# Kernel optimization log

Hardware: AMD Instinct MI355X
Metric: run time of the kernel (lower is better)

## Reference

```python
import jax, jax.numpy as jnp
import numpy as np

E = 192      # embed_dim
DI = 384     # d_inner = 2*E (mamba default expand=2)
S = 16       # d_state
R = 12       # dt_rank = ceil(E/16)
DEPTH = 4
STRIDE = 4
P = 400      # num_patches = 1600/4
NC = 20
BATCH = 32
EPS = 1e-5


def _rmsnorm(x, w):
    x = x.astype(jnp.float32)
    return x * jax.lax.rsqrt(jnp.mean(x * x, axis=-1, keepdims=True) + EPS) * w


def _mamba_mixer(h, in_w, cw, cb, xpw, dtw, dtb, a_log, d_skip, ow):
    # h: [B, L, E]
    Bsz, Ln, _ = h.shape
    xz = jnp.einsum('ble,de->bld', h, in_w)            # [B,L,2*DI]
    xm, z = xz[..., :DI], xz[..., DI:]
    # causal depthwise conv1d, kernel 4 (left pad 3, truncate to L)
    xp = jnp.pad(xm, ((0, 0), (3, 0), (0, 0)))
    xc = sum(xp[:, k:k + Ln, :] * cw[:, k] for k in range(4)) + cb
    xc = jax.nn.silu(xc)
    xdb = jnp.einsum('bld,rd->blr', xc, xpw)           # [B,L,R+2S]
    dt = jax.nn.softplus(jnp.einsum('blr,dr->bld', xdb[..., :R], dtw) + dtb)
    Bm = xdb[..., R:R + S]
    Cm = xdb[..., R + S:]
    A = -jnp.exp(a_log)                                # [DI,S]

    def step(hst, inp):
        dt_t, b_t, c_t, u_t = inp                      # [B,DI],[B,S],[B,S],[B,DI]
        dA = jnp.exp(dt_t[:, :, None] * A)             # [B,DI,S]
        hst = dA * hst + (dt_t * u_t)[:, :, None] * b_t[:, None, :]
        y_t = jnp.einsum('bdn,bn->bd', hst, c_t)
        return hst, y_t

    h0 = jnp.zeros((Bsz, DI, S), xc.dtype)
    xs = (dt.transpose(1, 0, 2), Bm.transpose(1, 0, 2), Cm.transpose(1, 0, 2), xc.transpose(1, 0, 2))
    _, ys = jax.lax.scan(step, h0, xs)
    y = ys.transpose(1, 0, 2) + xc * d_skip
    y = y * jax.nn.silu(z)
    return jnp.einsum('bld,ed->ble', y, ow)


def _forward(imgs, patch_w, patch_b, cls_token, pos_embed, cnn_w, cnn_b, norm_w,
             in_proj_w, conv_w, conv_b, x_proj_w, dt_proj_w, dt_proj_b, A_log, D,
             out_proj_w, norm_f_w, head_w, head_b):
    Bsz = imgs.shape[0]
    # StrideEmbed: conv1d kernel=stride=4 == reshape + matmul
    x = imgs.reshape(Bsz, P, STRIDE)
    x = jnp.einsum('blk,ek->ble', x, patch_w[:, 0, :]) + patch_b   # [B,P,E]
    x = x + pos_embed[:, :-1, :]
    # depthwise conv1d k=3 pad=1 over length
    xp = jnp.pad(x, ((0, 0), (1, 1), (0, 0)))
    x = sum(xp[:, k:k + P, :] * cnn_w[:, 0, k] for k in range(3)) + cnn_b
    cls = cls_token + pos_embed[:, -1, :]                           # [1,1,E]
    x = jnp.concatenate([x, jnp.broadcast_to(cls, (Bsz, 1, E))], axis=1)  # [B,401,E]

    hidden = x
    residual = None
    for i in range(DEPTH):
        residual = hidden if residual is None else residual + hidden
        hn = _rmsnorm(residual, norm_w[i])
        hidden = _mamba_mixer(hn, in_proj_w[i], conv_w[i], conv_b[i], x_proj_w[i],
                              dt_proj_w[i], dt_proj_b[i], A_log[i], D[i], out_proj_w[i])
    out = _rmsnorm(hidden + residual, norm_f_w)
    v_sem = out[:, -1, :]
    return v_sem @ head_w.T + head_b


def setup_inputs() -> dict:
    key = jax.random.key(0)
    ks = jax.random.split(key, 12)
    n = lambda k, shp, s=0.02: jax.random.normal(k, shp, dtype=jnp.float32) * s
    return {
        'imgs': jax.random.normal(ks[0], (BATCH, 1, 40, 40), jnp.float32),
        'patch_w': n(ks[1], (E, 1, STRIDE), 0.3),
        'patch_b': jnp.zeros((E,), jnp.float32),
        'cls_token': n(ks[2], (1, 1, E)),
        'pos_embed': n(ks[3], (1, P + 1, E)),
        'cnn_w': n(ks[4], (E, 1, 3), 0.3),
        'cnn_b': jnp.zeros((E,), jnp.float32),
        'norm_w': jnp.ones((DEPTH, E), jnp.float32),
        'in_proj_w': n(ks[5], (DEPTH, 2 * DI, E), 0.05),
        'conv_w': n(ks[6], (DEPTH, DI, 4), 0.3),
        'conv_b': jnp.zeros((DEPTH, DI), jnp.float32),
        'x_proj_w': n(ks[7], (DEPTH, R + 2 * S, DI), 0.05),
        'dt_proj_w': n(ks[8], (DEPTH, DI, R), 0.3),
        'dt_proj_b': jnp.log(jnp.expm1(jax.random.uniform(ks[9], (DEPTH, DI), minval=0.001, maxval=0.1))),
        'A_log': jnp.log(jnp.broadcast_to(jnp.arange(1, S + 1, dtype=jnp.float32), (DEPTH, DI, S))),
        'D': jnp.ones((DEPTH, DI), jnp.float32),
        'out_proj_w': n(ks[10], (DEPTH, E, DI), 0.05),
        'norm_f_w': jnp.ones((E,), jnp.float32),
        'head_w': n(ks[11], (NC, E)),
        'head_b': jnp.zeros((NC,), jnp.float32),
    }


def reference(imgs, patch_w, patch_b, cls_token, pos_embed, cnn_w, cnn_b, norm_w,
              in_proj_w, conv_w, conv_b, x_proj_w, dt_proj_w, dt_proj_b, A_log, D,
              out_proj_w, norm_f_w, head_w, head_b):
    return _forward(imgs, patch_w, patch_b, cls_token, pos_embed, cnn_w, cnn_b, norm_w,
                    in_proj_w, conv_w, conv_b, x_proj_w, dt_proj_w, dt_proj_b, A_log, D,
                    out_proj_w, norm_f_w, head_w, head_b)
```

## Files before the change

kernel.cpp:

```cpp
#include <hip/hip_runtime.h>
#include <math.h>

#define E 192
#define DI 384
#define S 16
#define R 12
#define DEPTH 4
#define P 400
#define NC 20
#define BATCH 32
#define L 401
#define NTOK (BATCH * L)
#define CH 64
#define NCH 7

using short8 = __attribute__((ext_vector_type(8))) short;
using float4v = __attribute__((ext_vector_type(4))) float;

__device__ __forceinline__ float siluf(float x) {
    return x / (1.f + __expf(-x));
}
__device__ __forceinline__ float softplusf(float x) {
    return (x > 20.f) ? x : log1pf(__expf(x));
}
__device__ __forceinline__ unsigned short f2bf(float x) {
    unsigned int u = __float_as_uint(x);
    unsigned int r = 0x7fffu + ((u >> 16) & 1u);
    return (unsigned short)((u + r) >> 16);
}

__global__ void k_embed(const float* __restrict__ imgs, const float* __restrict__ patch_w,
                        const float* __restrict__ patch_b, const float* __restrict__ cls_token,
                        const float* __restrict__ pos_embed, const float* __restrict__ cnn_w,
                        const float* __restrict__ cnn_b, float* __restrict__ resid) {
    int idx = blockIdx.x * blockDim.x + threadIdx.x;
    if (idx >= NTOK * E) return;
    int e = idx % E;
    int bl = idx / E;
    int l = bl % L;
    int b = bl / L;
    float out;
    if (l == P) {
        out = cls_token[e] + pos_embed[(size_t)P * E + e];
    } else {
        float w0 = patch_w[e * 4 + 0], w1 = patch_w[e * 4 + 1];
        float w2 = patch_w[e * 4 + 2], w3 = patch_w[e * 4 + 3];
        float pb = patch_b[e];
        const float* ib = imgs + (size_t)b * 1600;
        auto xe = [&](int ll) -> float {
            const float* ip = ib + ll * 4;
            return ip[0] * w0 + ip[1] * w1 + ip[2] * w2 + ip[3] * w3 + pb +
                   pos_embed[(size_t)ll * E + e];
        };
        float c0 = cnn_w[e * 3 + 0], c1 = cnn_w[e * 3 + 1], c2 = cnn_w[e * 3 + 2];
        float acc = cnn_b[e] + xe(l) * c1;
        if (l > 0) acc += xe(l - 1) * c0;
        if (l < P - 1) acc += xe(l + 1) * c2;
        out = acc;
    }
    resid[idx] = out;
}

template <bool ADD>
__global__ void k_rmsnorm(const float* __restrict__ hidden, float* __restrict__ resid,
                          unsigned short* __restrict__ hn, const float* __restrict__ w) {
    int wave = blockIdx.x * (blockDim.x >> 6) + (threadIdx.x >> 6);
    int lane = threadIdx.x & 63;
    if (wave >= NTOK) return;
    size_t base = (size_t)wave * E;
    float v[3];
    float ss = 0.f;
#pragma unroll
    for (int j = 0; j < 3; j++) {
        int e = lane + j * 64;
        float r = resid[base + e];
        if (ADD) {
            r += hidden[base + e];
            resid[base + e] = r;
        }
        v[j] = r;
        ss += r * r;
    }
#pragma unroll
    for (int off = 32; off > 0; off >>= 1) ss += __shfl_xor(ss, off, 64);
    float scale = rsqrtf(ss * (1.f / (float)E) + 1e-5f);
#pragma unroll
    for (int j = 0; j < 3; j++) {
        int e = lane + j * 64;
        hn[base + e] = f2bf(v[j] * scale * w[e]);
    }
}

__global__ void k_cvt(const float* __restrict__ src, unsigned short* __restrict__ dst, int n) {
    int idx = blockIdx.x * blockDim.x + threadIdx.x;
    if (idx < n) dst[idx] = f2bf(src[idx]);
}

__global__ __launch_bounds__(256) void k_gemm_bf16(const unsigned short* __restrict__ A,
                                                   const unsigned short* __restrict__ W,
                                                   float* __restrict__ C, int M, int N, int K) {
    constexpr int BM = 128, BN = 64, BK = 64, PADK = BK + 8;
    __shared__ unsigned short As[BM][PADK];
    __shared__ unsigned short Bs[BN][PADK];
    int tid = threadIdx.x;
    int m0 = blockIdx.y * BM, n0 = blockIdx.x * BN;
    int wave = tid >> 6, lane = tid & 63;
    int row16 = lane & 15, quad = lane >> 4;
    int wm0 = (wave >> 1) * 64, wn0 = (wave & 1) * 32;

    float4v acc[4][2];
#pragma unroll
    for (int i = 0; i < 4; i++)
#pragma unroll
        for (int j = 0; j < 2; j++) acc[i][j] = (float4v){0.f, 0.f, 0.f, 0.f};

    for (int k0 = 0; k0 < K; k0 += BK) {
#pragma unroll
        for (int p = 0; p < 4; p++) {
            int idx = (p * 256 + tid) * 8;
            int row = idx / BK, col = idx % BK;
            int gm = m0 + row;
            short8 v;
            if (gm < M)
                v = *(const short8*)&A[(size_t)gm * K + k0 + col];
            else
                v = (short8)0;
            *(short8*)&As[row][col] = v;
        }
#pragma unroll
        for (int p = 0; p < 2; p++) {
            int idx = (p * 256 + tid) * 8;
            int row = idx / BK, col = idx % BK;
            int gn = n0 + row;
            short8 v;
            if (gn < N)
                v = *(const short8*)&W[(size_t)gn * K + k0 + col];
            else
                v = (short8)0;
            *(short8*)&Bs[row][col] = v;
        }
        __syncthreads();
#pragma unroll
        for (int kk = 0; kk < BK; kk += 32) {
            int koff = kk + quad * 8;
            short8 af[4], bfr[2];
#pragma unroll
            for (int i = 0; i < 4; i++)
                af[i] = *(const short8*)&As[wm0 + i * 16 + row16][koff];
#pragma unroll
            for (int j = 0; j < 2; j++)
                bfr[j] = *(const short8*)&Bs[wn0 + j * 16 + row16][koff];
#pragma unroll
            for (int i = 0; i < 4; i++)
#pragma unroll
                for (int j = 0; j < 2; j++)
                    acc[i][j] = __builtin_amdgcn_mfma_f32_16x16x32_bf16(af[i], bfr[j],
                                                                        acc[i][j], 0, 0, 0);
        }
        __syncthreads();
    }
#pragma unroll
    for (int i = 0; i < 4; i++) {
#pragma unroll
        for (int j = 0; j < 2; j++) {
#pragma unroll
            for (int r = 0; r < 4; r++) {
                int m = m0 + wm0 + i * 16 + quad * 4 + r;
                int n = n0 + wn0 + j * 16 + row16;
                if (m < M && n < N) C[(size_t)m * N + n] = acc[i][j][r];
            }
        }
    }
}

__global__ void k_conv(const float* __restrict__ xz, const float* __restrict__ cw,
                       const float* __restrict__ cb, float* __restrict__ xc,
                       unsigned short* __restrict__ xc_bf) {
    int idx = blockIdx.x * blockDim.x + threadIdx.x;
    if (idx >= NTOK * DI) return;
    int d = idx % DI;
    int bl = idx / DI;
    int l = bl % L;
    int b = bl / L;
    const float* base = xz + (size_t)b * L * (2 * DI) + d;
    float acc = cb[d];
#pragma unroll
    for (int k = 0; k < 4; k++) {
        int ll = l - 3 + k;
        if (ll >= 0) acc += base[(size_t)ll * (2 * DI)] * cw[d * 4 + k];
    }
    float v = siluf(acc);
    xc[idx] = v;
    xc_bf[idx] = f2bf(v);
}

__global__ void k_dtproj(const float* __restrict__ xdb, const float* __restrict__ dtw,
                         const float* __restrict__ dtb, float* __restrict__ dt) {
    int idx = blockIdx.x * blockDim.x + threadIdx.x;
    if (idx >= NTOK * DI) return;
    int d = idx % DI;
    int tok = idx / DI;
    const float* xr = xdb + (size_t)tok * 44;
    const float* wr = dtw + (size_t)d * R;
    float acc = dtb[d];
#pragma unroll
    for (int r = 0; r < R; r++) acc += xr[r] * wr[r];
    dt[idx] = softplusf(acc);
}

__global__ void k_scanA(const float* __restrict__ dt, const float* __restrict__ xc,
                        const float* __restrict__ xdb, const float* __restrict__ A_log,
                        float* __restrict__ hend, float* __restrict__ dtsum) {
    int d = threadIdx.x;
    int ch = blockIdx.x;
    int b = blockIdx.y;
    int t0 = ch * CH;
    int t1 = min(t0 + CH, L);
    float a[S];
#pragma unroll
    for (int n = 0; n < S; n++) a[n] = -__expf(A_log[d * S + n]);
    float h[S] = {};
    float dts = 0.f;
    for (int t = t0; t < t1; t++) {
        size_t tok = (size_t)b * L + t;
        float dtv = dt[tok * DI + d];
        float u = xc[tok * DI + d];
        dts += dtv;
        float dtu = dtv * u;
        const float* bv = xdb + tok * 44 + R;
#pragma unroll
        for (int n = 0; n < S; n++) {
            float dA = __expf(dtv * a[n]);
            h[n] = dA * h[n] + dtu * bv[n];
        }
    }
    size_t o = (((size_t)b * NCH + ch) * DI + d) * S;
#pragma unroll
    for (int n = 0; n < S; n++) hend[o + n] = h[n];
    dtsum[((size_t)b * NCH + ch) * DI + d] = dts;
}

__global__ void k_scanB(const float* __restrict__ hend, const float* __restrict__ dtsum,
                        const float* __restrict__ A_log, float* __restrict__ hinit) {
    int idx = blockIdx.x * blockDim.x + threadIdx.x;
    if (idx >= BATCH * DI) return;
    int d = idx % DI;
    int b = idx / DI;
    float a[S];
#pragma unroll
    for (int n = 0; n < S; n++) a[n] = -__expf(A_log[d * S + n]);
    float h[S] = {};
    for (int ch = 0; ch < NCH; ch++) {
        size_t o = (((size_t)b * NCH + ch) * DI + d) * S;
#pragma unroll
        for (int n = 0; n < S; n++) hinit[o + n] = h[n];
        float dts = dtsum[((size_t)b * NCH + ch) * DI + d];
#pragma unroll
        for (int n = 0; n < S; n++) h[n] = __expf(dts * a[n]) * h[n] + hend[o + n];
    }
}

__global__ void k_scanC(const float* __restrict__ xz, const float* __restrict__ xc,
                        const float* __restrict__ xdb, const float* __restrict__ A_log,
                        const float* __restrict__ Dskip, const float* __restrict__ hinit,
                        const float* __restrict__ dt, unsigned short* __restrict__ y_bf) {
    int d = threadIdx.x;
    int ch = blockIdx.x;
    int b = blockIdx.y;
    int t0 = ch * CH;
    int t1 = min(t0 + CH, L);
    float a[S];
#pragma unroll
    for (int n = 0; n < S; n++) a[n] = -__expf(A_log[d * S + n]);
    float h[S];
    size_t o = (((size_t)b * NCH + ch) * DI + d) * S;
#pragma unroll
    for (int n = 0; n < S; n++) h[n] = hinit[o + n];
    float dsk = Dskip[d];
    for (int t = t0; t < t1; t++) {
        size_t tok = (size_t)b * L + t;
        float dtv = dt[tok * DI + d];
        float u = xc[tok * DI + d];
        float z = xz[tok * (2 * DI) + DI + d];
        float dtu = dtv * u;
        const float* bv = xdb + tok * 44 + R;
        const float* cv = xdb + tok * 44 + R + S;
        float y = 0.f;
#pragma unroll
        for (int n = 0; n < S; n++) {
            float dA = __expf(dtv * a[n]);
            h[n] = dA * h[n] + dtu * bv[n];
            y += h[n] * cv[n];
        }
        y += u * dsk;
        y_bf[tok * DI + d] = f2bf(y * siluf(z));
    }
}

__global__ void k_head(const float* __restrict__ resid, const float* __restrict__ hidden,
                       const float* __restrict__ norm_f_w, const float* __restrict__ head_w,
                       const float* __restrict__ head_b, float* __restrict__ out) {
    __shared__ float v[E];
    int b = blockIdx.x;
    int lane = threadIdx.x;
    size_t base = ((size_t)b * L + P) * E;
    float loc[3];
    float ss = 0.f;
#pragma unroll
    for (int j = 0; j < 3; j++) {
        int e = lane + j * 64;
        float x = resid[base + e] + hidden[base + e];
        loc[j] = x;
        ss += x * x;
    }
#pragma unroll
    for (int off = 32; off > 0; off >>= 1) ss += __shfl_xor(ss, off, 64);
    float scale = rsqrtf(ss * (1.f / (float)E) + 1e-5f);
#pragma unroll
    for (int j = 0; j < 3; j++) {
        int e = lane + j * 64;
        v[e] = loc[j] * scale * norm_f_w[e];
    }
    __syncthreads();
    if (lane < NC) {
        float acc = head_b[lane];
        for (int e = 0; e < E; e++) acc += v[e] * head_w[lane * E + e];
        out[b * NC + lane] = acc;
    }
}

extern "C" void kernel_launch(void* const* d_in, const int* in_sizes, int n_in,
                              void* d_out, int out_size, void* d_ws, size_t ws_size,
                              hipStream_t stream) {
    const float* imgs      = (const float*)d_in[0];
    const float* patch_w   = (const float*)d_in[1];
    const float* patch_b   = (const float*)d_in[2];
    const float* cls_token = (const float*)d_in[3];
    const float* pos_embed = (const float*)d_in[4];
    const float* cnn_w     = (const float*)d_in[5];
    const float* cnn_b     = (const float*)d_in[6];
    const float* norm_w    = (const float*)d_in[7];
    const float* in_proj_w = (const float*)d_in[8];
    const float* conv_w    = (const float*)d_in[9];
    const float* conv_b    = (const float*)d_in[10];
    const float* x_proj_w  = (const float*)d_in[11];
    const float* dt_proj_w = (const float*)d_in[12];
    const float* dt_proj_b = (const float*)d_in[13];
    const float* A_log     = (const float*)d_in[14];
    const float* Dskip     = (const float*)d_in[15];
    const float* out_proj_w= (const float*)d_in[16];
    const float* norm_f_w  = (const float*)d_in[17];
    const float* head_w    = (const float*)d_in[18];
    const float* head_b    = (const float*)d_in[19];

    float* ws = (float*)d_ws;
    size_t off = 0;
    float* resid  = ws + off; off += (size_t)NTOK * E;
    float* hidden = ws + off; off += (size_t)NTOK * E;
    float* xz     = ws + off; off += (size_t)NTOK * 2 * DI;
    float* xc     = ws + off; off += (size_t)NTOK * DI;
    float* xdb    = ws + off; off += (size_t)NTOK * 44;
    float* dt     = ws + off; off += (size_t)NTOK * DI;
    float* hend   = ws + off; off += (size_t)BATCH * NCH * DI * S;
    float* hinit  = ws + off; off += (size_t)BATCH * NCH * DI * S;
    float* dtsum  = ws + off; off += (size_t)BATCH * NCH * DI;
    unsigned short* bf_buf = (unsigned short*)(ws + off); off += (size_t)NTOK * DI / 2;
    unsigned short* w_in  = (unsigned short*)(ws + off); off += (size_t)DEPTH * 2 * DI * E / 2;
    unsigned short* w_x   = (unsigned short*)(ws + off); off += (size_t)DEPTH * 44 * DI / 2 + 8;
    unsigned short* w_out = (unsigned short*)(ws + off); off += (size_t)DEPTH * E * DI / 2;

    unsigned short* hn_bf = bf_buf;
    unsigned short* xc_bf = bf_buf;
    unsigned short* y_bf  = bf_buf;

    {
        int n1 = DEPTH * 2 * DI * E;
        k_cvt<<<(n1 + 255) / 256, 256, 0, stream>>>(in_proj_w, w_in, n1);
        int n2 = DEPTH * 44 * DI;
        k_cvt<<<(n2 + 255) / 256, 256, 0, stream>>>(x_proj_w, w_x, n2);
        int n3 = DEPTH * E * DI;
        k_cvt<<<(n3 + 255) / 256, 256, 0, stream>>>(out_proj_w, w_out, n3);
    }

    k_embed<<<(NTOK * E) / 256, 256, 0, stream>>>(imgs, patch_w, patch_b, cls_token,
                                                  pos_embed, cnn_w, cnn_b, resid);

    for (int i = 0; i < DEPTH; i++) {
        if (i == 0)
            k_rmsnorm<false><<<NTOK / 4, 256, 0, stream>>>(hidden, resid, hn_bf, norm_w + i * E);
        else
            k_rmsnorm<true><<<NTOK / 4, 256, 0, stream>>>(hidden, resid, hn_bf, norm_w + i * E);

        {
            dim3 g((2 * DI) / 64, (NTOK + 127) / 128);
            k_gemm_bf16<<<g, 256, 0, stream>>>(hn_bf, w_in + (size_t)i * 2 * DI * E, xz,
                                               NTOK, 2 * DI, E);
        }
        k_conv<<<(NTOK * DI) / 256, 256, 0, stream>>>(xz, conv_w + (size_t)i * DI * 4,
                                                      conv_b + (size_t)i * DI, xc, xc_bf);
        {
            dim3 g(1, (NTOK + 127) / 128);
            k_gemm_bf16<<<g, 256, 0, stream>>>(xc_bf, w_x + (size_t)i * 44 * DI, xdb,
                                               NTOK, 44, DI);
        }
        k_dtproj<<<(NTOK * DI) / 256, 256, 0, stream>>>(xdb, dt_proj_w + (size_t)i * DI * R,
                                                        dt_proj_b + (size_t)i * DI, dt);
        {
            dim3 g(NCH, BATCH);
            k_scanA<<<g, DI, 0, stream>>>(dt, xc, xdb, A_log + (size_t)i * DI * S, hend, dtsum);
            k_scanB<<<(BATCH * DI + 255) / 256, 256, 0, stream>>>(
                hend, dtsum, A_log + (size_t)i * DI * S, hinit);
            k_scanC<<<g, DI, 0, stream>>>(xz, xc, xdb, A_log + (size_t)i * DI * S,
                                          Dskip + (size_t)i * DI, hinit, dt, y_bf);
        }
        {
            dim3 g(E / 64, (NTOK + 127) / 128);
            k_gemm_bf16<<<g, 256, 0, stream>>>(y_bf, w_out + (size_t)i * E * DI, hidden,
                                               NTOK, E, DI);
        }
    }

    k_head<<<BATCH, 64, 0, stream>>>(resid, hidden, norm_f_w, head_w, head_b, (float*)d_out);
}
```

Before: 864.3 us.

## Restructure chunked scan to compute local outputs and fix up with closed-form carry

Fuses the dt projection and softplus into the first scan pass. That pass now also emits each chunk's local output with zero initial state plus a running dt cumsum. The second full recurrence pass is replaced by an elementwise fixup kernel that adds C·exp(A·cumdt)·h_init. Chunks are halved to raise parallelism, A is precomputed once, and the GEMM gets templated M-tile sizes so the narrow projections launch more blocks. This trades a sequential pass for extra memory traffic on the ylocal and dtcum buffers and some exp recomputation.

```diff
diff --git a/kernel.cpp b/kernel.cpp
--- a/kernel.cpp
+++ b/kernel.cpp
@@ -11,8 +11,8 @@
 #define BATCH 32
 #define L 401
 #define NTOK (BATCH * L)
-#define CH 64
-#define NCH 7
+#define CH 32
+#define NCH 13
 
 using short8 = __attribute__((ext_vector_type(8))) short;
 using float4v = __attribute__((ext_vector_type(4))) float;
@@ -96,27 +96,34 @@
     if (idx < n) dst[idx] = f2bf(src[idx]);
 }
 
+__global__ void k_preA(const float* __restrict__ A_log, float* __restrict__ negA, int n) {
+    int idx = blockIdx.x * blockDim.x + threadIdx.x;
+    if (idx < n) negA[idx] = -__expf(A_log[idx]);
+}
+
+template <int BM>
 __global__ __launch_bounds__(256) void k_gemm_bf16(const unsigned short* __restrict__ A,
                                                    const unsigned short* __restrict__ W,
                                                    float* __restrict__ C, int M, int N, int K) {
-    constexpr int BM = 128, BN = 64, BK = 64, PADK = BK + 8;
+    constexpr int BN = 64, BK = 64, PADK = BK + 8;
+    constexpr int MT = BM / 32;
     __shared__ unsigned short As[BM][PADK];
     __shared__ unsigned short Bs[BN][PADK];
     int tid = threadIdx.x;
     int m0 = blockIdx.y * BM, n0 = blockIdx.x * BN;
     int wave = tid >> 6, lane = tid & 63;
     int row16 = lane & 15, quad = lane >> 4;
-    int wm0 = (wave >> 1) * 64, wn0 = (wave & 1) * 32;
-
-    float4v acc[4][2];
-#pragma unroll
-    for (int i = 0; i < 4; i++)
+    int wm0 = (wave >> 1) * (BM / 2), wn0 = (wave & 1) * 32;
+
+    float4v acc[MT][2];
+#pragma unroll
+    for (int i = 0; i < MT; i++)
 #pragma unroll
         for (int j = 0; j < 2; j++) acc[i][j] = (float4v){0.f, 0.f, 0.f, 0.f};
 
     for (int k0 = 0; k0 < K; k0 += BK) {
 #pragma unroll
-        for (int p = 0; p < 4; p++) {
+        for (int p = 0; p < MT; p++) {
             int idx = (p * 256 + tid) * 8;
             int row = idx / BK, col = idx % BK;
             int gm = m0 + row;
@@ -143,15 +150,15 @@
 #pragma unroll
         for (int kk = 0; kk < BK; kk += 32) {
             int koff = kk + quad * 8;
-            short8 af[4], bfr[2];
-#pragma unroll
-            for (int i = 0; i < 4; i++)
+            short8 af[MT], bfr[2];
+#pragma unroll
+            for (int i = 0; i < MT; i++)
                 af[i] = *(const short8*)&As[wm0 + i * 16 + row16][koff];
 #pragma unroll
             for (int j = 0; j < 2; j++)
                 bfr[j] = *(const short8*)&Bs[wn0 + j * 16 + row16][koff];
 #pragma unroll
-            for (int i = 0; i < 4; i++)
+            for (int i = 0; i < MT; i++)
 #pragma unroll
                 for (int j = 0; j < 2; j++)
                     acc[i][j] = __builtin_amdgcn_mfma_f32_16x16x32_bf16(af[i], bfr[j],
@@ -160,7 +167,7 @@
         __syncthreads();
     }
 #pragma unroll
-    for (int i = 0; i < 4; i++) {
+    for (int i = 0; i < MT; i++) {
 #pragma unroll
         for (int j = 0; j < 2; j++) {
 #pragma unroll
@@ -194,23 +201,11 @@
     xc_bf[idx] = f2bf(v);
 }
 
-__global__ void k_dtproj(const float* __restrict__ xdb, const float* __restrict__ dtw,
-                         const float* __restrict__ dtb, float* __restrict__ dt) {
-    int idx = blockIdx.x * blockDim.x + threadIdx.x;
-    if (idx >= NTOK * DI) return;
-    int d = idx % DI;
-    int tok = idx / DI;
-    const float* xr = xdb + (size_t)tok * 44;
-    const float* wr = dtw + (size_t)d * R;
-    float acc = dtb[d];
-#pragma unroll
-    for (int r = 0; r < R; r++) acc += xr[r] * wr[r];
-    dt[idx] = softplusf(acc);
-}
-
-__global__ void k_scanA(const float* __restrict__ dt, const float* __restrict__ xc,
-                        const float* __restrict__ xdb, const float* __restrict__ A_log,
-                        float* __restrict__ hend, float* __restrict__ dtsum) {
+__global__ void k_scanA(const float* __restrict__ xc, const float* __restrict__ xdb,
+                        const float* __restrict__ negA, const float* __restrict__ dtw,
+                        const float* __restrict__ dtb, const float* __restrict__ Dskip,
+                        float* __restrict__ ylocal, float* __restrict__ dtcum,
+                        float* __restrict__ hend) {
     int d = threadIdx.x;
     int ch = blockIdx.x;
     int b = blockIdx.y;
@@ -218,83 +213,84 @@
     int t1 = min(t0 + CH, L);
     float a[S];
 #pragma unroll
-    for (int n = 0; n < S; n++) a[n] = -__expf(A_log[d * S + n]);
+    for (int n = 0; n < S; n++) a[n] = negA[d * S + n];
+    float wdt[R];
+#pragma unroll
+    for (int r = 0; r < R; r++) wdt[r] = dtw[d * R + r];
+    float bias = dtb[d];
+    float dsk = Dskip[d];
     float h[S] = {};
     float dts = 0.f;
     for (int t = t0; t < t1; t++) {
         size_t tok = (size_t)b * L + t;
-        float dtv = dt[tok * DI + d];
+        const float* row = xdb + tok * 44;
+        float dtacc = bias;
+#pragma unroll
+        for (int r = 0; r < R; r++) dtacc += row[r] * wdt[r];
+        float dtv = softplusf(dtacc);
+        dts += dtv;
         float u = xc[tok * DI + d];
-        dts += dtv;
         float dtu = dtv * u;
-        const float* bv = xdb + tok * 44 + R;
+        float y = u * dsk;
 #pragma unroll
         for (int n = 0; n < S; n++) {
             float dA = __expf(dtv * a[n]);
-            h[n] = dA * h[n] + dtu * bv[n];
-        }
+            h[n] = dA * h[n] + dtu * row[R + n];
+            y += h[n] * row[R + S + n];
+        }
+        ylocal[tok * DI + d] = y;
+        dtcum[tok * DI + d] = dts;
     }
     size_t o = (((size_t)b * NCH + ch) * DI + d) * S;
 #pragma unroll
     for (int n = 0; n < S; n++) hend[o + n] = h[n];
-    dtsum[((size_t)b * NCH + ch) * DI + d] = dts;
-}
-
-__global__ void k_scanB(const float* __restrict__ hend, const float* __restrict__ dtsum,
-                        const float* __restrict__ A_log, float* __restrict__ hinit) {
+}
+
+__global__ void k_scanB(const float* __restrict__ hend, const float* __restrict__ dtcum,
+                        const float* __restrict__ negA, float* __restrict__ hinit) {
     int idx = blockIdx.x * blockDim.x + threadIdx.x;
     if (idx >= BATCH * DI) return;
     int d = idx % DI;
     int b = idx / DI;
     float a[S];
 #pragma unroll
-    for (int n = 0; n < S; n++) a[n] = -__expf(A_log[d * S + n]);
+    for (int n = 0; n < S; n++) a[n] = negA[d * S + n];
     float h[S] = {};
     for (int ch = 0; ch < NCH; ch++) {
         size_t o = (((size_t)b * NCH + ch) * DI + d) * S;
 #pragma unroll
         for (int n = 0; n < S; n++) hinit[o + n] = h[n];
-        float dts = dtsum[((size_t)b * NCH + ch) * DI + d];
+        int tlast = min(ch * CH + CH, L) - 1;
+        float dts = dtcum[((size_t)b * L + tlast) * DI + d];
 #pragma unroll
         for (int n = 0; n < S; n++) h[n] = __expf(dts * a[n]) * h[n] + hend[o + n];
     }
 }
 
-__global__ void k_scanC(const float* __restrict__ xz, const float* __restrict__ xc,
-                        const float* __restrict__ xdb, const float* __restrict__ A_log,
-                        const float* __restrict__ Dskip, const float* __restrict__ hinit,
-                        const float* __restrict__ dt, unsigned short* __restrict__ y_bf) {
-    int d = threadIdx.x;
-    int ch = blockIdx.x;
-    int b = blockIdx.y;
-    int t0 = ch * CH;
-    int t1 = min(t0 + CH, L);
-    float a[S];
-#pragma unroll
-    for (int n = 0; n < S; n++) a[n] = -__expf(A_log[d * S + n]);
-    float h[S];
-    size_t o = (((size_t)b * NCH + ch) * DI + d) * S;
-#pragma unroll
-    for (int n = 0; n < S; n++) h[n] = hinit[o + n];
-    float dsk = Dskip[d];
-    for (int t = t0; t < t1; t++) {
-        size_t tok = (size_t)b * L + t;
-        float dtv = dt[tok * DI + d];
-        float u = xc[tok * DI + d];
-        float z = xz[tok * (2 * DI) + DI + d];
-        float dtu = dtv * u;
-        const float* bv = xdb + tok * 44 + R;
-        const float* cv = xdb + tok * 44 + R + S;
-        float y = 0.f;
-#pragma unroll
-        for (int n = 0; n < S; n++) {
-            float dA = __expf(dtv * a[n]);
-            h[n] = dA * h[n] + dtu * bv[n];
-            y += h[n] * cv[n];
-        }
-        y += u * dsk;
-        y_bf[tok * DI + d] = f2bf(y * siluf(z));
-    }
+__global__ void k_fixup(const float* __restrict__ xz, const float* __restrict__ xdb,
+                        const float* __restrict__ negA, const float* __restrict__ hinit,
+                        const float* __restrict__ ylocal, const float* __restrict__ dtcum,
+                        unsigned short* __restrict__ y_bf) {
+    int idx = blockIdx.x * blockDim.x + threadIdx.x;
+    if (idx >= NTOK * DI) return;
+    int d = idx % DI;
+    int tok = idx / DI;
+    int l = tok % L;
+    int b = tok / L;
+    int ch = l / CH;
+    float y = ylocal[idx];
+    if (ch != 0) {
+        float dts = dtcum[idx];
+        const float* h0 = hinit + (((size_t)b * NCH + ch) * DI + d) * S;
+        const float* an = negA + d * S;
+        const float* cv = xdb + (size_t)tok * 44 + R + S;
+        float corr = 0.f;
+#pragma unroll
+        for (int n = 0; n < S; n++) corr += cv[n] * __expf(an[n] * dts) * h0[n];
+        y += corr;
+    }
+    float z = xz[(size_t)tok * (2 * DI) + DI + d];
+    y_bf[idx] = f2bf(y * siluf(z));
 }
 
 __global__ void k_head(const float* __restrict__ resid, const float* __restrict__ hidden,
@@ -360,13 +356,14 @@
     float* xz     = ws + off; off += (size_t)NTOK * 2 * DI;
     float* xc     = ws + off; off += (size_t)NTOK * DI;
     float* xdb    = ws + off; off += (size_t)NTOK * 44;
-    float* dt     = ws + off; off += (size_t)NTOK * DI;
+    float* ylocal = ws + off; off += (size_t)NTOK * DI;
+    float* dtcum  = ws + off; off += (size_t)NTOK * DI;
     float* hend   = ws + off; off += (size_t)BATCH * NCH * DI * S;
     float* hinit  = ws + off; off += (size_t)BATCH * NCH * DI * S;
-    float* dtsum  = ws + off; off += (size_t)BATCH * NCH * DI;
+    float* negA   = ws + off; off += (size_t)DEPTH * DI * S;
     unsigned short* bf_buf = (unsigned short*)(ws + off); off += (size_t)NTOK * DI / 2;
     unsigned short* w_in  = (unsigned short*)(ws + off); off += (size_t)DEPTH * 2 * DI * E / 2;
-    unsigned short* w_x   = (unsigned short*)(ws + off); off += (size_t)DEPTH * 44 * DI / 2 + 8;
+    unsigned short* w_x   = (unsigned short*)(ws + off); off += (size_t)DEPTH * 44 * DI / 2 + 16;
     unsigned short* w_out = (unsigned short*)(ws + off); off += (size_t)DEPTH * E * DI / 2;
 
     unsigned short* hn_bf = bf_buf;
@@ -380,6 +377,8 @@
         k_cvt<<<(n2 + 255) / 256, 256, 0, stream>>>(x_proj_w, w_x, n2);
         int n3 = DEPTH * E * DI;
         k_cvt<<<(n3 + 255) / 256, 256, 0, stream>>>(out_proj_w, w_out, n3);
+        int n4 = DEPTH * DI * S;
+        k_preA<<<(n4 + 255) / 256, 256, 0, stream>>>(A_log, negA, n4);
     }
 
     k_embed<<<(NTOK * E) / 256, 256, 0, stream>>>(imgs, patch_w, patch_b, cls_token,
@@ -393,30 +392,30 @@
 
         {
             dim3 g((2 * DI) / 64, (NTOK + 127) / 128);
-            k_gemm_bf16<<<g, 256, 0, stream>>>(hn_bf, w_in + (size_t)i * 2 * DI * E, xz,
-                                               NTOK, 2 * DI, E);
+            k_gemm_bf16<128><<<g, 256, 0, stream>>>(hn_bf, w_in + (size_t)i * 2 * DI * E, xz,
+                                                    NTOK, 2 * DI, E);
         }
         k_conv<<<(NTOK * DI) / 256, 256, 0, stream>>>(xz, conv_w + (size_t)i * DI * 4,
                                                       conv_b + (size_t)i * DI, xc, xc_bf);
         {
-            dim3 g(1, (NTOK + 127) / 128);
-            k_gemm_bf16<<<g, 256, 0, stream>>>(xc_bf, w_x + (size_t)i * 44 * DI, xdb,
-                                               NTOK, 44, DI);
-        }
-        k_dtproj<<<(NTOK * DI) / 256, 256, 0, stream>>>(xdb, dt_proj_w + (size_t)i * DI * R,
-                                                        dt_proj_b + (size_t)i * DI, dt);
+            dim3 g(1, NTOK / 32);
+            k_gemm_bf16<32><<<g, 256, 0, stream>>>(xc_bf, w_x + (size_t)i * 44 * DI, xdb,
+                                                   NTOK, 44, DI);
+        }
         {
+            const float* nA = negA + (size_t)i * DI * S;
             dim3 g(NCH, BATCH);
-            k_scanA<<<g, DI, 0, stream>>>(dt, xc, xdb, A_log + (size_t)i * DI * S, hend, dtsum);
-            k_scanB<<<(BATCH * DI + 255) / 256, 256, 0, stream>>>(
-                hend, dtsum, A_log + (size_t)i * DI * S, hinit);
-            k_scanC<<<g, DI, 0, stream>>>(xz, xc, xdb, A_log + (size_t)i * DI * S,
-                                          Dskip + (size_t)i * DI, hinit, dt, y_bf);
+            k_scanA<<<g, DI, 0, stream>>>(xc, xdb, nA, dt_proj_w + (size_t)i * DI * R,
+                                          dt_proj_b + (size_t)i * DI, Dskip + (size_t)i * DI,
+                                          ylocal, dtcum, hend);
+            k_scanB<<<(BATCH * DI + 255) / 256, 256, 0, stream>>>(hend, dtcum, nA, hinit);
+            k_fixup<<<(NTOK * DI + 255) / 256, 256, 0, stream>>>(xz, xdb, nA, hinit,
+                                                                 ylocal, dtcum, y_bf);
         }
         {
-            dim3 g(E / 64, (NTOK + 127) / 128);
-            k_gemm_bf16<<<g, 256, 0, stream>>>(y_bf, w_out + (size_t)i * E * DI, hidden,
-                                               NTOK, E, DI);
+            dim3 g(E / 64, (NTOK + 63) / 64);
+            k_gemm_bf16<64><<<g, 256, 0, stream>>>(y_bf, w_out + (size_t)i * E * DI, hidden,
+                                                   NTOK, E, DI);
         }
     }
 
```

After: 877.4 us. Within noise of the previous version (+1.5%).
